# Kernel tuning notes

Hardware: AMD Instinct MI355X
Metric: run time of the kernel (lower is better)

The kernel has to match this reference:

```python
import jax, jax.numpy as jnp
import numpy as np

DIM = 256
HEADS = 8

def conv1x1(x, W, b):
    # x: [b,c,h,w], W: [o,c], b: [o]
    return jnp.einsum('oc,bchw->bohw', W, x) + b[None, :, None, None]

def setup_inputs() -> dict:
    key = jax.random.key(0)
    ks = jax.random.split(key, 16)
    B, C, H, Wd = 8, DIM, 96, 96
    s = 1.0 / np.sqrt(C)
    inp = {
        'x': jax.random.normal(ks[0], (B, C, H, Wd), jnp.float32),
        'y': jax.random.normal(ks[1], (B, C, H, Wd), jnp.float32),
        'z': jax.random.normal(ks[2], (B, C, H, Wd), jnp.float32),
        'W_qr': jax.random.normal(ks[3], (C // 2, C), jnp.float32) * s,
        'b_qr': jnp.zeros((C // 2,), jnp.float32),
        'W_qd': jax.random.normal(ks[4], (C // 2, C), jnp.float32) * s,
        'b_qd': jnp.zeros((C // 2,), jnp.float32),
        'W_kf': jax.random.normal(ks[5], (C, C), jnp.float32) * s,
        'b_kf': jnp.zeros((C,), jnp.float32),
        'W_vf': jax.random.normal(ks[6], (C, C), jnp.float32) * s,
        'b_vf': jnp.zeros((C,), jnp.float32),
        'W_cat': jax.random.normal(ks[7], (C, C), jnp.float32) * s,
        'b_cat': jnp.zeros((C,), jnp.float32),
        'W_proj': jax.random.normal(ks[8], (C, C), jnp.float32) * s,
        'b_proj': jnp.zeros((C,), jnp.float32),
        'temperature': jnp.ones((HEADS, 1, 1), jnp.float32),
    }
    return inp

def reference(x, y, z, W_qr, b_qr, W_qd, b_qd, W_kf, b_kf, W_vf, b_vf,
              W_cat, b_cat, W_proj, b_proj, temperature):
    b, c, h, w = x.shape
    hw = h * w
    ch = c // HEADS  # channels per head

    q_r = conv1x1(x, W_qr, b_qr)
    q_d = conv1x1(y, W_qd, b_qd)
    k_f = conv1x1(z, W_kf, b_kf)
    v_f = conv1x1(z, W_vf, b_vf)
    q = conv1x1(jnp.concatenate([q_r, q_d], axis=1), W_cat, b_cat)

    def to_heads(t):  # [b, head*ch, h, w] -> [b, head, ch, hw]
        return t.reshape(b, HEADS, ch, hw)

    q = to_heads(q)
    k = to_heads(k_f)
    v = to_heads(v_f)

    # L2-normalize along spatial axis (eps=1e-12 as in F.normalize)
    q = q / jnp.maximum(jnp.linalg.norm(q, axis=-1, keepdims=True), 1e-12)
    k = k / jnp.maximum(jnp.linalg.norm(k, axis=-1, keepdims=True), 1e-12)

    # channel attention: [b,head,ch,ch]
    attn = jnp.einsum('bhcn,bhdn->bhcd', q, k) * temperature[None]
    attn = jax.nn.softmax(attn, axis=-1)
    out = jnp.einsum('bhcd,bhdn->bhcn', attn, v)  # [b,head,ch,hw]
    out = out.reshape(b, c, h, w)
    return conv1x1(out, W_proj, b_proj) + z
```

## Files before the change

### kernel.cpp

```cpp
#include <hip/hip_runtime.h>
#include <hip/hip_bf16.h>

#define HW 9216
#define CDIM 256
#define NBATCH 8
#define NHEADS 8

typedef __bf16 bf16x8 __attribute__((ext_vector_type(8)));
typedef float f32x4 __attribute__((ext_vector_type(4)));

__device__ inline unsigned short f2bf(float f) {
    unsigned int u = __builtin_bit_cast(unsigned int, f);
    u = (u + 0x7FFF + ((u >> 16) & 1)) >> 16;
    return (unsigned short)u;
}
__device__ inline float bf2f(unsigned short s) {
    unsigned int u = ((unsigned int)s) << 16;
    return __builtin_bit_cast(float, u);
}
__device__ inline unsigned int pk2(float a, float b) {
    return (unsigned int)f2bf(a) | ((unsigned int)f2bf(b) << 16);
}
__device__ inline float ldx(const float* p) { return *p; }
__device__ inline float ldx(const unsigned short* p) { return bf2f(*p); }
__device__ inline void stx(float* p, float v) { *p = v; }
__device__ inline void stx(unsigned short* p, float v) { *p = f2bf(v); }

__global__ void fuse_wq(const float* __restrict__ W_cat, const float* __restrict__ W_qr,
                        const float* __restrict__ W_qd, const float* __restrict__ b_qr,
                        const float* __restrict__ b_qd, const float* __restrict__ b_cat,
                        unsigned short* __restrict__ Wq, float* __restrict__ bq) {
    int o = blockIdx.x;
    int c = threadIdx.x;
    float ax = 0.f, ay = 0.f;
    for (int i = 0; i < 128; ++i) {
        ax += W_cat[o * 256 + i] * W_qr[i * 256 + c];
        ay += W_cat[o * 256 + 128 + i] * W_qd[i * 256 + c];
    }
    Wq[o * 512 + c] = f2bf(ax);
    Wq[o * 512 + 256 + c] = f2bf(ay);
    if (c == 0) {
        float s = b_cat[o];
        for (int i = 0; i < 128; ++i)
            s += W_cat[o * 256 + i] * b_qr[i] + W_cat[o * 256 + 128 + i] * b_qd[i];
        bq[o] = s;
    }
}

__global__ void cvt_w(const float* __restrict__ a, const float* __restrict__ b,
                      unsigned short* __restrict__ oa, unsigned short* __restrict__ ob) {
    int i = blockIdx.x * 256 + threadIdx.x;
    oa[i] = f2bf(a[i]);
    ob[i] = f2bf(b[i]);
}

template <typename TX, typename TOut>
__global__ __launch_bounds__(256) void gemm_mfma(
    const unsigned short* __restrict__ A, int a_bs, int Ktot,
    const TX* __restrict__ X0, const TX* __restrict__ X1,
    const float* __restrict__ bias, const float* __restrict__ resid,
    TOut* __restrict__ Out) {
    const int b = blockIdx.z;
    const int n0 = blockIdx.x * 128;
    const int m0 = blockIdx.y * 128;
    const int tid = threadIdx.x;
    const int lane = tid & 63;
    const int wid = tid >> 6;
    const int wm = (wid >> 1) * 64;
    const int wn = (wid & 1) * 64;
    const int l15 = lane & 15;
    const int quad = lane >> 4;

    __shared__ __align__(16) unsigned short Bs[4 * 128 * 8];

    const unsigned short* Ab = A + (size_t)b * a_bs;
    const TX* Xb0 = X0 + (size_t)b * CDIM * HW;
    const TX* Xb1 = X1 ? X1 + (size_t)b * CDIM * HW : nullptr;

    f32x4 acc[4][4] = {};

    const int sn = tid & 127;
    const int sq0 = (tid >> 7) * 2;

    for (int k0 = 0; k0 < Ktot; k0 += 32) {
        const TX* Xp = (k0 < 256) ? Xb0 : Xb1;
        const int k0r = k0 & 255;

#pragma unroll
        for (int qq = 0; qq < 2; ++qq) {
            int q = sq0 + qq;
            const TX* src = Xp + (size_t)(k0r + q * 8) * HW + n0 + sn;
            float f[8];
#pragma unroll
            for (int j = 0; j < 8; ++j) f[j] = ldx(src + (size_t)j * HW);
            uint4 pk;
            pk.x = pk2(f[0], f[1]);
            pk.y = pk2(f[2], f[3]);
            pk.z = pk2(f[4], f[5]);
            pk.w = pk2(f[6], f[7]);
            *(uint4*)&Bs[(q * 128 + sn) * 8] = pk;
        }

        bf16x8 af[4];
#pragma unroll
        for (int mi = 0; mi < 4; ++mi)
            af[mi] = *(const bf16x8*)(Ab + (size_t)(m0 + wm + mi * 16 + l15) * Ktot + k0 + quad * 8);

        __syncthreads();

        bf16x8 bfr[4];
#pragma unroll
        for (int nj = 0; nj < 4; ++nj)
            bfr[nj] = *(const bf16x8*)&Bs[(quad * 128 + wn + nj * 16 + l15) * 8];

#pragma unroll
        for (int mi = 0; mi < 4; ++mi)
#pragma unroll
            for (int nj = 0; nj < 4; ++nj)
                acc[mi][nj] = __builtin_amdgcn_mfma_f32_16x16x32_bf16(af[mi], bfr[nj], acc[mi][nj], 0, 0, 0);

        __syncthreads();
    }

#pragma unroll
    for (int mi = 0; mi < 4; ++mi) {
#pragma unroll
        for (int r = 0; r < 4; ++r) {
            int m = m0 + wm + mi * 16 + quad * 4 + r;
            float bv = bias[m];
#pragma unroll
            for (int nj = 0; nj < 4; ++nj) {
                int n = n0 + wn + nj * 16 + l15;
                size_t off = ((size_t)b * CDIM + m) * HW + n;
                float v = acc[mi][nj][r] + bv;
                if (resid) v += resid[off];
                stx(&Out[off], v);
            }
        }
    }
}

__global__ __launch_bounds__(256) void gram_kernel(
    const unsigned short* __restrict__ q, const unsigned short* __restrict__ k,
    float* __restrict__ G, float* __restrict__ sqq, float* __restrict__ sqk) {
    const int nc = blockIdx.x;
    const int h = blockIdx.y, b = blockIdx.z;
    const int t = threadIdx.x;

    __shared__ float qs[32][128];
    __shared__ float ks[32][129];

    size_t base = ((size_t)b * CDIM + h * 32) * HW + nc * 128;
#pragma unroll
    for (int i = 0; i < 16; ++i) {
        int idx = i * 256 + t;
        int row = idx >> 7, col = idx & 127;
        qs[row][col] = bf2f(q[base + (size_t)row * HW + col]);
        ks[row][col] = bf2f(k[base + (size_t)row * HW + col]);
    }
    __syncthreads();

    const int d = t & 31;
    const int cb = t >> 5;
    float acc[4] = {0.f, 0.f, 0.f, 0.f};
    for (int n = 0; n < 128; ++n) {
        float kv = ks[d][n];
#pragma unroll
        for (int p = 0; p < 4; ++p) acc[p] += qs[cb + 8 * p][n] * kv;
    }

    float* Gp = G + (size_t)(b * 8 + h) * 32 * 32;
#pragma unroll
    for (int p = 0; p < 4; ++p) atomicAdd(&Gp[(cb + 8 * p) * 32 + d], acc[p]);

    if (t < 64) {
        int c = t & 31;
        float sq = 0.f;
        if (t < 32) {
            for (int n = 0; n < 128; ++n) { float v = qs[c][n]; sq += v * v; }
            atomicAdd(&sqq[(b * 8 + h) * 32 + c], sq);
        } else {
            for (int n = 0; n < 128; ++n) { float v = ks[c][n]; sq += v * v; }
            atomicAdd(&sqk[(b * 8 + h) * 32 + c], sq);
        }
    }
}

__global__ __launch_bounds__(1024) void softmax_kernel(
    const float* __restrict__ G, const float* __restrict__ sqq,
    const float* __restrict__ sqk, const float* __restrict__ temp,
    float* __restrict__ A) {
    int bh = blockIdx.x;
    int h = bh & 7;
    int c = threadIdx.y, d = threadIdx.x;
    float nq = fmaxf(sqrtf(sqq[bh * 32 + c]), 1e-12f);
    float nk = fmaxf(sqrtf(sqk[bh * 32 + d]), 1e-12f);
    float v = G[(size_t)(bh * 32 + c) * 32 + d] / (nq * nk) * temp[h];
    float m = v;
    for (int s = 16; s > 0; s >>= 1) m = fmaxf(m, __shfl_xor(m, s, 32));
    float e = __expf(v - m);
    float sum = e;
    for (int s = 16; s > 0; s >>= 1) sum += __shfl_xor(sum, s, 32);
    A[(size_t)(bh * 32 + c) * 32 + d] = e / sum;
}

__global__ __launch_bounds__(256) void build_m(const float* __restrict__ W_proj,
                                               const float* __restrict__ A,
                                               unsigned short* __restrict__ M) {
    int o = blockIdx.x;
    int b = blockIdx.y;
    int t = threadIdx.x;
    int h = t >> 5, d = t & 31;
    const float* Ab = A + (size_t)(b * 8 + h) * 32 * 32;
    float acc = 0.f;
    for (int c = 0; c < 32; ++c)
        acc += W_proj[o * 256 + h * 32 + c] * Ab[c * 32 + d];
    M[((size_t)b * 256 + o) * 256 + t] = f2bf(acc);
}

extern "C" void kernel_launch(void* const* d_in, const int* in_sizes, int n_in,
                              void* d_out, int out_size, void* d_ws, size_t ws_size,
                              hipStream_t stream) {
    const float* x = (const float*)d_in[0];
    const float* y = (const float*)d_in[1];
    const float* z = (const float*)d_in[2];
    const float* W_qr = (const float*)d_in[3];
    const float* b_qr = (const float*)d_in[4];
    const float* W_qd = (const float*)d_in[5];
    const float* b_qd = (const float*)d_in[6];
    const float* W_kf = (const float*)d_in[7];
    const float* b_kf = (const float*)d_in[8];
    const float* W_vf = (const float*)d_in[9];
    const float* b_vf = (const float*)d_in[10];
    const float* W_cat = (const float*)d_in[11];
    const float* b_cat = (const float*)d_in[12];
    const float* W_proj = (const float*)d_in[13];
    const float* b_proj = (const float*)d_in[14];
    const float* temp = (const float*)d_in[15];
    float* out = (float*)d_out;

    char* ws = (char*)d_ws;
    const size_t NT = (size_t)NBATCH * CDIM * HW;
    unsigned short* qb = (unsigned short*)ws;
    unsigned short* kb = qb + NT;
    unsigned short* vb = kb + NT;
    char* p = (char*)(vb + NT);
    unsigned short* Wq = (unsigned short*)p;  p += 256 * 512 * 2;
    unsigned short* Wk = (unsigned short*)p;  p += 256 * 256 * 2;
    unsigned short* Wv = (unsigned short*)p;  p += 256 * 256 * 2;
    float* bq  = (float*)p;                   p += 1024;
    float* G   = (float*)p;                   p += 64 * 32 * 32 * 4;
    float* sqq = (float*)p;                   p += 2048 * 4;
    float* sqk = (float*)p;                   p += 2048 * 4;
    float* Aat = (float*)p;                   p += 64 * 32 * 32 * 4;
    unsigned short* Mb = (unsigned short*)p;  p += (size_t)8 * 256 * 256 * 2;

    hipMemsetAsync(G, 0, 262144 + 8192 + 8192, stream);

    fuse_wq<<<256, 256, 0, stream>>>(W_cat, W_qr, W_qd, b_qr, b_qd, b_cat, Wq, bq);
    cvt_w<<<256, 256, 0, stream>>>(W_kf, W_vf, Wk, Wv);

    dim3 gg(HW / 128, CDIM / 128, NBATCH);
    gemm_mfma<float, unsigned short><<<gg, 256, 0, stream>>>(Wq, 0, 512, x, y, bq, nullptr, qb);
    gemm_mfma<float, unsigned short><<<gg, 256, 0, stream>>>(Wk, 0, 256, z, nullptr, b_kf, nullptr, kb);
    gemm_mfma<float, unsigned short><<<gg, 256, 0, stream>>>(Wv, 0, 256, z, nullptr, b_vf, nullptr, vb);

    gram_kernel<<<dim3(HW / 128, NHEADS, NBATCH), 256, 0, stream>>>(qb, kb, G, sqq, sqk);
    softmax_kernel<<<64, dim3(32, 32), 0, stream>>>(G, sqq, sqk, temp, Aat);
    build_m<<<dim3(256, 8), 256, 0, stream>>>(W_proj, Aat, Mb);

    gemm_mfma<unsigned short, float><<<gg, 256, 0, stream>>>(Mb, 256 * 256, 256, vb, nullptr, b_proj, z, out);
}
```

Before: 521.5 us.

## Double-buffer GEMM tiles, merge K/V projections, and vectorize gram loads

The GEMM kernel now uses two shared-memory buffers and register prefetch, so global loads for the next K-tile are issued before the MFMA work on the current one, and one barrier per step is removed. The K and V projections, which both read z, are merged into a single GEMM with a stacked 512x256 weight and a split output offset. This removes one launch and lets the two projections share their z tile loads. The gram kernel loads bf16 values four at a time and spreads the squared-norm reductions across all threads instead of only 64. These changes cost extra registers and shared memory, which may lower occupancy.

Result: slower. 634.5 us (+21.7%).

```diff
diff --git a/kernel.cpp b/kernel.cpp
--- a/kernel.cpp
+++ b/kernel.cpp
@@ -47,11 +47,14 @@
     }
 }
 
-__global__ void cvt_w(const float* __restrict__ a, const float* __restrict__ b,
-                      unsigned short* __restrict__ oa, unsigned short* __restrict__ ob) {
-    int i = blockIdx.x * 256 + threadIdx.x;
-    oa[i] = f2bf(a[i]);
-    ob[i] = f2bf(b[i]);
+__global__ void cvt_wkv(const float* __restrict__ W_kf, const float* __restrict__ W_vf,
+                        const float* __restrict__ b_kf, const float* __restrict__ b_vf,
+                        unsigned short* __restrict__ Wkv, float* __restrict__ bkv) {
+    int o = blockIdx.x;
+    int c = threadIdx.x;
+    const float* src = (o < 256) ? &W_kf[(size_t)o * 256] : &W_vf[(size_t)(o - 256) * 256];
+    Wkv[(size_t)o * 256 + c] = f2bf(src[c]);
+    if (c == 0) bkv[o] = (o < 256) ? b_kf[o] : b_vf[o - 256];
 }
 
 template <typename TX, typename TOut>
@@ -59,7 +62,7 @@
     const unsigned short* __restrict__ A, int a_bs, int Ktot,
     const TX* __restrict__ X0, const TX* __restrict__ X1,
     const float* __restrict__ bias, const float* __restrict__ resid,
-    TOut* __restrict__ Out) {
+    TOut* __restrict__ Out, size_t split_off) {
     const int b = blockIdx.z;
     const int n0 = blockIdx.x * 128;
     const int m0 = blockIdx.y * 128;
@@ -71,7 +74,7 @@
     const int l15 = lane & 15;
     const int quad = lane >> 4;
 
-    __shared__ __align__(16) unsigned short Bs[4 * 128 * 8];
+    __shared__ __align__(16) unsigned short Bs[2][4 * 128 * 8];
 
     const unsigned short* Ab = A + (size_t)b * a_bs;
     const TX* Xb0 = X0 + (size_t)b * CDIM * HW;
@@ -82,44 +85,68 @@
     const int sn = tid & 127;
     const int sq0 = (tid >> 7) * 2;
 
-    for (int k0 = 0; k0 < Ktot; k0 += 32) {
-        const TX* Xp = (k0 < 256) ? Xb0 : Xb1;
-        const int k0r = k0 & 255;
-
+    int arow[4];
+#pragma unroll
+    for (int mi = 0; mi < 4; ++mi)
+        arow[mi] = (m0 + wm + mi * 16 + l15) * Ktot + quad * 8;
+
+    const int nkt = Ktot >> 5;
+
+    float fA[2][8], fB[2][8];
+    bf16x8 af[4], af2[4];
+
+#pragma unroll
+    for (int qq = 0; qq < 2; ++qq) {
+        const TX* src = Xb0 + (size_t)((sq0 + qq) * 8) * HW + n0 + sn;
+#pragma unroll
+        for (int j = 0; j < 8; ++j) fA[qq][j] = ldx(src + (size_t)j * HW);
+    }
+#pragma unroll
+    for (int mi = 0; mi < 4; ++mi) af[mi] = *(const bf16x8*)(Ab + arow[mi]);
+
+    auto step = [&](int kt, float (&fc)[2][8], float (&fn)[2][8],
+                    bf16x8 (&ac)[4], bf16x8 (&an)[4], int bsel) {
 #pragma unroll
         for (int qq = 0; qq < 2; ++qq) {
-            int q = sq0 + qq;
-            const TX* src = Xp + (size_t)(k0r + q * 8) * HW + n0 + sn;
-            float f[8];
-#pragma unroll
-            for (int j = 0; j < 8; ++j) f[j] = ldx(src + (size_t)j * HW);
             uint4 pk;
-            pk.x = pk2(f[0], f[1]);
-            pk.y = pk2(f[2], f[3]);
-            pk.z = pk2(f[4], f[5]);
-            pk.w = pk2(f[6], f[7]);
-            *(uint4*)&Bs[(q * 128 + sn) * 8] = pk;
+            pk.x = pk2(fc[qq][0], fc[qq][1]);
+            pk.y = pk2(fc[qq][2], fc[qq][3]);
+            pk.z = pk2(fc[qq][4], fc[qq][5]);
+            pk.w = pk2(fc[qq][6], fc[qq][7]);
+            *(uint4*)&Bs[bsel][((sq0 + qq) * 128 + sn) * 8] = pk;
         }
-
-        bf16x8 af[4];
+        __syncthreads();
+
+        if (kt + 1 < nkt) {
+            int k0n = (kt + 1) * 32;
+            const TX* Xp = (k0n < 256) ? Xb0 : Xb1;
+            int k0r = k0n & 255;
+#pragma unroll
+            for (int qq = 0; qq < 2; ++qq) {
+                const TX* src = Xp + (size_t)(k0r + (sq0 + qq) * 8) * HW + n0 + sn;
+#pragma unroll
+                for (int j = 0; j < 8; ++j) fn[qq][j] = ldx(src + (size_t)j * HW);
+            }
+#pragma unroll
+            for (int mi = 0; mi < 4; ++mi)
+                an[mi] = *(const bf16x8*)(Ab + arow[mi] + k0n);
+        }
+
+        bf16x8 bfr[4];
+#pragma unroll
+        for (int nj = 0; nj < 4; ++nj)
+            bfr[nj] = *(const bf16x8*)&Bs[bsel][(quad * 128 + wn + nj * 16 + l15) * 8];
+
 #pragma unroll
         for (int mi = 0; mi < 4; ++mi)
-            af[mi] = *(const bf16x8*)(Ab + (size_t)(m0 + wm + mi * 16 + l15) * Ktot + k0 + quad * 8);
-
-        __syncthreads();
-
-        bf16x8 bfr[4];
-#pragma unroll
-        for (int nj = 0; nj < 4; ++nj)
-            bfr[nj] = *(const bf16x8*)&Bs[(quad * 128 + wn + nj * 16 + l15) * 8];
-
-#pragma unroll
-        for (int mi = 0; mi < 4; ++mi)
 #pragma unroll
             for (int nj = 0; nj < 4; ++nj)
-                acc[mi][nj] = __builtin_amdgcn_mfma_f32_16x16x32_bf16(af[mi], bfr[nj], acc[mi][nj], 0, 0, 0);
-
-        __syncthreads();
+                acc[mi][nj] = __builtin_amdgcn_mfma_f32_16x16x32_bf16(ac[mi], bfr[nj], acc[mi][nj], 0, 0, 0);
+    };
+
+    for (int kt = 0; kt < nkt; kt += 2) {
+        step(kt, fA, fB, af, af2, 0);
+        step(kt + 1, fB, fA, af2, af, 1);
     }
 
 #pragma unroll
@@ -128,10 +155,11 @@
         for (int r = 0; r < 4; ++r) {
             int m = m0 + wm + mi * 16 + quad * 4 + r;
             float bv = bias[m];
+            size_t base_off = ((m >= 256) ? split_off : 0) + ((size_t)b * CDIM + (m & 255)) * HW;
 #pragma unroll
             for (int nj = 0; nj < 4; ++nj) {
                 int n = n0 + wn + nj * 16 + l15;
-                size_t off = ((size_t)b * CDIM + m) * HW + n;
+                size_t off = base_off + n;
                 float v = acc[mi][nj][r] + bv;
                 if (resid) v += resid[off];
                 stx(&Out[off], v);
@@ -152,11 +180,15 @@
 
     size_t base = ((size_t)b * CDIM + h * 32) * HW + nc * 128;
 #pragma unroll
-    for (int i = 0; i < 16; ++i) {
+    for (int i = 0; i < 4; ++i) {
         int idx = i * 256 + t;
-        int row = idx >> 7, col = idx & 127;
-        qs[row][col] = bf2f(q[base + (size_t)row * HW + col]);
-        ks[row][col] = bf2f(k[base + (size_t)row * HW + col]);
+        int row = idx >> 5, c4 = (idx & 31) * 4;
+        ushort4 qv = *(const ushort4*)&q[base + (size_t)row * HW + c4];
+        ushort4 kv = *(const ushort4*)&k[base + (size_t)row * HW + c4];
+        qs[row][c4 + 0] = bf2f(qv.x); qs[row][c4 + 1] = bf2f(qv.y);
+        qs[row][c4 + 2] = bf2f(qv.z); qs[row][c4 + 3] = bf2f(qv.w);
+        ks[row][c4 + 0] = bf2f(kv.x); ks[row][c4 + 1] = bf2f(kv.y);
+        ks[row][c4 + 2] = bf2f(kv.z); ks[row][c4 + 3] = bf2f(kv.w);
     }
     __syncthreads();
 
@@ -173,16 +205,16 @@
 #pragma unroll
     for (int p = 0; p < 4; ++p) atomicAdd(&Gp[(cb + 8 * p) * 32 + d], acc[p]);
 
-    if (t < 64) {
-        int c = t & 31;
-        float sq = 0.f;
-        if (t < 32) {
-            for (int n = 0; n < 128; ++n) { float v = qs[c][n]; sq += v * v; }
-            atomicAdd(&sqq[(b * 8 + h) * 32 + c], sq);
-        } else {
-            for (int n = 0; n < 128; ++n) { float v = ks[c][n]; sq += v * v; }
-            atomicAdd(&sqk[(b * 8 + h) * 32 + c], sq);
+    {
+        int c = t & 31, part = t >> 5;
+        float s1 = 0.f, s2 = 0.f;
+#pragma unroll
+        for (int n = part * 16; n < part * 16 + 16; ++n) {
+            float a = qs[c][n]; s1 += a * a;
+            float e = ks[c][n]; s2 += e * e;
         }
+        atomicAdd(&sqq[(b * 8 + h) * 32 + c], s1);
+        atomicAdd(&sqk[(b * 8 + h) * 32 + c], s2);
     }
 }
 
@@ -245,29 +277,30 @@
     unsigned short* kb = qb + NT;
     unsigned short* vb = kb + NT;
     char* p = (char*)(vb + NT);
-    unsigned short* Wq = (unsigned short*)p;  p += 256 * 512 * 2;
-    unsigned short* Wk = (unsigned short*)p;  p += 256 * 256 * 2;
-    unsigned short* Wv = (unsigned short*)p;  p += 256 * 256 * 2;
-    float* bq  = (float*)p;                   p += 1024;
-    float* G   = (float*)p;                   p += 64 * 32 * 32 * 4;
-    float* sqq = (float*)p;                   p += 2048 * 4;
-    float* sqk = (float*)p;                   p += 2048 * 4;
-    float* Aat = (float*)p;                   p += 64 * 32 * 32 * 4;
-    unsigned short* Mb = (unsigned short*)p;  p += (size_t)8 * 256 * 256 * 2;
+    unsigned short* Wq  = (unsigned short*)p;  p += 256 * 512 * 2;
+    unsigned short* Wkv = (unsigned short*)p;  p += 512 * 256 * 2;
+    float* bq  = (float*)p;                    p += 1024;
+    float* bkv = (float*)p;                    p += 2048;
+    float* G   = (float*)p;                    p += 64 * 32 * 32 * 4;
+    float* sqq = (float*)p;                    p += 2048 * 4;
+    float* sqk = (float*)p;                    p += 2048 * 4;
+    float* Aat = (float*)p;                    p += 64 * 32 * 32 * 4;
+    unsigned short* Mb = (unsigned short*)p;   p += (size_t)8 * 256 * 256 * 2;
 
     hipMemsetAsync(G, 0, 262144 + 8192 + 8192, stream);
 
     fuse_wq<<<256, 256, 0, stream>>>(W_cat, W_qr, W_qd, b_qr, b_qd, b_cat, Wq, bq);
-    cvt_w<<<256, 256, 0, stream>>>(W_kf, W_vf, Wk, Wv);
-
-    dim3 gg(HW / 128, CDIM / 128, NBATCH);
-    gemm_mfma<float, unsigned short><<<gg, 256, 0, stream>>>(Wq, 0, 512, x, y, bq, nullptr, qb);
-    gemm_mfma<float, unsigned short><<<gg, 256, 0, stream>>>(Wk, 0, 256, z, nullptr, b_kf, nullptr, kb);
-    gemm_mfma<float, unsigned short><<<gg, 256, 0, stream>>>(Wv, 0, 256, z, nullptr, b_vf, nullptr, vb);
+    cvt_wkv<<<512, 256, 0, stream>>>(W_kf, W_vf, b_kf, b_vf, Wkv, bkv);
+
+    gemm_mfma<float, unsigned short><<<dim3(HW / 128, 2, NBATCH), 256, 0, stream>>>(
+        Wq, 0, 512, x, y, bq, nullptr, qb, 0);
+    gemm_mfma<float, unsigned short><<<dim3(HW / 128, 4, NBATCH), 256, 0, stream>>>(
+        Wkv, 0, 256, z, nullptr, bkv, nullptr, kb, NT);
 
     gram_kernel<<<dim3(HW / 128, NHEADS, NBATCH), 256, 0, stream>>>(qb, kb, G, sqq, sqk);
     softmax_kernel<<<64, dim3(32, 32), 0, stream>>>(G, sqq, sqk, temp, Aat);
     build_m<<<dim3(256, 8), 256, 0, stream>>>(W_proj, Aat, Mb);
 
-    gemm_mfma<unsigned short, float><<<gg, 256, 0, stream>>>(Mb, 256 * 256, 256, vb, nullptr, b_proj, z, out);
-}
+    gemm_mfma<unsigned short, float><<<dim3(HW / 128, 2, NBATCH), 256, 0, stream>>>(
+        Mb, 256 * 256, 256, vb, nullptr, b_proj, z, out, 0);
+}
```
